# Kernel optimization log

Measured on AMD Instinct MI355X. Metric: run time of the kernel, lower is better.

Reference implementation:

```python
import jax, jax.numpy as jnp
from jax import lax
import numpy as np

N = 10000      # nodes
E = 160000     # edges (avg degree 16)
IN = 128       # in_channels
H = 64         # hidden_channels
OUT = 112      # out_channels
L = 28         # num GENConv layers
LN_EPS = 1e-5
MSG_EPS = 1e-7   # GENConv adds eps after relu in message
SM_EPS = 1e-16   # PyG scatter-softmax denominator eps


def _ln(x, g, b):
    mu = jnp.mean(x, axis=-1, keepdims=True)
    var = jnp.mean(jnp.square(x - mu), axis=-1, keepdims=True)
    return (x - mu) * lax.rsqrt(var + LN_EPS) * g + b


def setup_inputs() -> dict:
    key = jax.random.key(0)
    ks = jax.random.split(key, 8)

    def w(k, shape, fan_in):
        return (jax.random.normal(k, shape, dtype=jnp.float32) / np.float32(np.sqrt(fan_in)))

    x = jax.random.normal(ks[0], (N, IN), dtype=jnp.float32)
    edge_index = jax.random.randint(ks[1], (2, E), 0, N, dtype=jnp.int32)

    inp = {
        "x": x,
        "edge_index": edge_index,
        # node encoder
        "enc_W": w(ks[2], (IN, H), IN),
        "enc_b": jnp.zeros((H,), jnp.float32),
        # per-layer DeepGCNLayer LayerNorm (res+ pre-norm)
        "ln_g": jnp.ones((L, H), jnp.float32),
        "ln_b": jnp.zeros((L, H), jnp.float32),
        # per-layer learnable softmax temperature t (init 1.0)
        "t": jnp.ones((L,), jnp.float32),
        # GENConv inner MLP: Linear(H,2H) -> LayerNorm -> ReLU -> Linear(2H,H)
        "W1": w(ks[3], (L, H, 2 * H), H),
        "b1": jnp.zeros((L, 2 * H), jnp.float32),
        "mlp_g": jnp.ones((L, 2 * H), jnp.float32),
        "mlp_b": jnp.zeros((L, 2 * H), jnp.float32),
        "W2": w(ks[4], (L, 2 * H, H), 2 * H),
        "b2": jnp.zeros((L, H), jnp.float32),
        # output head
        "head_W": w(ks[5], (H, OUT), H),
        "head_b": jnp.zeros((OUT,), jnp.float32),
    }
    return inp


def reference(x, edge_index, enc_W, enc_b, ln_g, ln_b, t, W1, b1,
              mlp_g, mlp_b, W2, b2, head_W, head_b):
    src, dst = edge_index[0], edge_index[1]
    n = x.shape[0]

    h = x @ enc_W + enc_b  # node encoder

    def layer(h, params):
        lg, lb, tt, w1, bb1, mg, mb, w2, bb2 = params
        # DeepGCNLayer 'res+': norm -> act -> (dropout: identity at eval) -> conv -> residual
        z = jax.nn.relu(_ln(h, lg, lb))  # [N,H]
        # GENConv message: relu(x_j) + eps   (no edge_attr)
        m = jax.nn.relu(z[src]) + MSG_EPS  # [E,H]
        # softmax aggregation per destination node, per channel, temperature t
        logits = m * tt
        mx = jax.ops.segment_max(logits, dst, num_segments=n)  # [N,H]
        mx = jnp.where(jnp.isfinite(mx), mx, 0.0)              # empty segments
        ex = jnp.exp(logits - mx[dst])
        den = jax.ops.segment_sum(ex, dst, num_segments=n)
        alpha = ex / (den[dst] + SM_EPS)
        agg = jax.ops.segment_sum(alpha * m, dst, num_segments=n)  # [N,H]
        # GENConv: out = mlp(x_r + aggr)
        out = agg + z
        u = jax.nn.relu(_ln(out @ w1 + bb1, mg, mb))
        u = u @ w2 + bb2
        return h + u, None  # residual

    h, _ = lax.scan(layer, h, (ln_g, ln_b, t, W1, b1, mlp_g, mlp_b, W2, b2))
    return h @ head_W + head_b  # [N,OUT]
```

## Files before the change

### kernel.cpp

```cpp
#include <hip/hip_runtime.h>

#define N_NODES 10000
#define N_EDGES 160000
#define IN_CH 128
#define H 64
#define H2 128
#define OUT_CH 112
#define NLAYERS 28

__global__ __launch_bounds__(256) void k_count(const int* __restrict__ ei, int* __restrict__ deg) {
  int e = blockIdx.x * 256 + threadIdx.x;
  atomicAdd(&deg[ei[N_EDGES + e]], 1);
}

__global__ __launch_bounds__(1024) void k_scan(const int* __restrict__ deg, int* __restrict__ offs) {
  __shared__ int sums[1024];
  constexpr int CH = 10;
  int t = threadIdx.x;
  int base = t * CH;
  int local[CH];
  int s = 0;
  #pragma unroll
  for (int i = 0; i < CH; i++) {
    int idx = base + i;
    int v = (idx < N_NODES) ? deg[idx] : 0;
    local[i] = s; s += v;
  }
  sums[t] = s;
  __syncthreads();
  for (int off = 1; off < 1024; off <<= 1) {
    int v = (t >= off) ? sums[t - off] : 0;
    __syncthreads();
    sums[t] += v;
    __syncthreads();
  }
  int prev = (t == 0) ? 0 : sums[t - 1];
  #pragma unroll
  for (int i = 0; i < CH; i++) {
    int idx = base + i;
    if (idx < N_NODES) offs[idx] = prev + local[i];
  }
  if (t == 1023) offs[N_NODES] = sums[1023];
}

__global__ __launch_bounds__(256) void k_fill(const int* __restrict__ ei, const int* __restrict__ offs,
                                              int* __restrict__ cur, int* __restrict__ csr) {
  int e = blockIdx.x * 256 + threadIdx.x;
  int d = ei[N_EDGES + e];
  int p = offs[d] + atomicAdd(&cur[d], 1);
  csr[p] = ei[e];
}

__global__ __launch_bounds__(256) void k_pack(const float* __restrict__ W1, const float* __restrict__ W2,
                                              float* __restrict__ W1P, float* __restrict__ W2P) {
  int l = blockIdx.x;
  const float* w1 = W1 + l * 8192; float* p1 = W1P + l * 8192;
  const float* w2 = W2 + l * 8192; float* p2 = W2P + l * 8192;
  int t = threadIdx.x;
  for (int i = t; i < 8192; i += 256) {
    int g = i >> 9, r = i & 511;
    int lane = r >> 3, j = (r >> 1) & 3, c = r & 1;
    p1[i] = w1[(4 * g + j) * H2 + lane * 2 + c];
  }
  for (int i = t; i < 8192; i += 256) {
    int g = i >> 8, r = i & 255;
    int lane = r >> 2, j = r & 3;
    p2[i] = w2[(4 * g + j) * H + lane];
  }
}

__global__ __launch_bounds__(256) void k_encoder(
    const float* __restrict__ x, const float* __restrict__ Wenc, const float* __restrict__ benc,
    const float* __restrict__ lng, const float* __restrict__ lnb,
    float* __restrict__ h, float* __restrict__ z) {
  __shared__ float Xs[8][IN_CH];
  int t = threadIdx.x;
  int tile = blockIdx.x * 8;
  {
    int r = t >> 5, c4 = t & 31;
    float4 v = ((const float4*)x)[(tile + r) * 32 + c4];
    *(float4*)&Xs[r][c4 * 4] = v;
  }
  __syncthreads();
  int lane = t & 63;
  int wave = __builtin_amdgcn_readfirstlane(t >> 6);
  int n0 = wave * 2;
  float b = benc[lane];
  float a0 = b, a1 = b;
  #pragma unroll
  for (int k = 0; k < IN_CH; k += 4) {
    float4 X0 = *(float4*)&Xs[n0][k];
    float4 X1 = *(float4*)&Xs[n0 + 1][k];
    float w0 = Wenc[(k + 0) * H + lane];
    float w1 = Wenc[(k + 1) * H + lane];
    float w2 = Wenc[(k + 2) * H + lane];
    float w3 = Wenc[(k + 3) * H + lane];
    a0 = fmaf(X0.x, w0, a0); a0 = fmaf(X0.y, w1, a0); a0 = fmaf(X0.z, w2, a0); a0 = fmaf(X0.w, w3, a0);
    a1 = fmaf(X1.x, w0, a1); a1 = fmaf(X1.y, w1, a1); a1 = fmaf(X1.z, w2, a1); a1 = fmaf(X1.w, w3, a1);
  }
  float g = lng[lane], bb = lnb[lane];
  #pragma unroll
  for (int i = 0; i < 2; i++) {
    float a = (i == 0) ? a0 : a1;
    float s = a, q = a * a;
    #pragma unroll
    for (int m = 1; m < 64; m <<= 1) { s += __shfl_xor(s, m); q += __shfl_xor(q, m); }
    float mu = s * (1.0f / 64.0f);
    float var = q * (1.0f / 64.0f) - mu * mu;
    float rs = rsqrtf(var + 1e-5f);
    int gn = tile + n0 + i;
    h[gn * H + lane] = a;
    z[gn * H + lane] = fmaxf(fmaf((a - mu) * rs, g, bb), 0.f);
  }
}

__global__ __launch_bounds__(256) void k_layer(
    const float* __restrict__ zc, float* __restrict__ zn, float* __restrict__ h,
    const int* __restrict__ offs, const int* __restrict__ csr,
    const float* __restrict__ tvec,
    const float* __restrict__ W1P, const float* __restrict__ b1,
    const float* __restrict__ mg, const float* __restrict__ mb,
    const float* __restrict__ W2P, const float* __restrict__ b2,
    const float* __restrict__ lngn, const float* __restrict__ lnbn,
    int l) {
  __shared__ float As[8][H];
  __shared__ float Us[8][H2];
  int t = threadIdx.x;
  int lane = t & 63;
  int wave = __builtin_amdgcn_readfirstlane(t >> 6);
  int nb0 = blockIdx.x * 8 + wave * 2;

  float tl = tvec[l] * 1.44269504088896340736f;
  #pragma unroll
  for (int i = 0; i < 2; i++) {
    int gn = nb0 + i;
    int e0 = offs[gn], e1 = offs[gn + 1];
    float d0 = 0.f, d1 = 0.f, d2 = 0.f, d3 = 0.f;
    float a0 = 0.f, a1 = 0.f, a2 = 0.f, a3 = 0.f;
    int e = e0;
    for (; e + 4 <= e1; e += 4) {
      int s0 = csr[e], s1 = csr[e + 1], s2 = csr[e + 2], s3 = csr[e + 3];
      float v0 = zc[s0 * H + lane] + 1e-7f;
      float v1 = zc[s1 * H + lane] + 1e-7f;
      float v2 = zc[s2 * H + lane] + 1e-7f;
      float v3 = zc[s3 * H + lane] + 1e-7f;
      float p0 = exp2f(v0 * tl), p1 = exp2f(v1 * tl);
      float p2 = exp2f(v2 * tl), p3 = exp2f(v3 * tl);
      d0 += p0; d1 += p1; d2 += p2; d3 += p3;
      a0 = fmaf(p0, v0, a0); a1 = fmaf(p1, v1, a1);
      a2 = fmaf(p2, v2, a2); a3 = fmaf(p3, v3, a3);
    }
    for (; e < e1; e++) {
      int s0 = csr[e];
      float v0 = zc[s0 * H + lane] + 1e-7f;
      float p0 = exp2f(v0 * tl);
      d0 += p0; a0 = fmaf(p0, v0, a0);
    }
    float den = (d0 + d1) + (d2 + d3);
    float acc = (a0 + a1) + (a2 + a3);
    As[wave * 2 + i][lane] = acc / (den + 1e-16f) + zc[gn * H + lane];
  }
  __syncthreads();

  {
    const float* W1Pl = W1P + (size_t)l * (H * H2);
    const float* b1l = b1 + l * H2;
    int c0 = lane * 2;
    float bb0 = b1l[c0], bb1 = b1l[c0 + 1];
    float u00 = bb0, u01 = bb1, u10 = bb0, u11 = bb1;
    #pragma unroll
    for (int g = 0; g < 16; g++) {
      float4 A0 = *(float4*)&As[wave * 2 + 0][g * 4];
      float4 A1 = *(float4*)&As[wave * 2 + 1][g * 4];
      float4 wa = *(const float4*)&W1Pl[g * 512 + lane * 8];
      float4 wb = *(const float4*)&W1Pl[g * 512 + lane * 8 + 4];
      u00 = fmaf(A0.x, wa.x, u00); u01 = fmaf(A0.x, wa.y, u01);
      u00 = fmaf(A0.y, wa.z, u00); u01 = fmaf(A0.y, wa.w, u01);
      u00 = fmaf(A0.z, wb.x, u00); u01 = fmaf(A0.z, wb.y, u01);
      u00 = fmaf(A0.w, wb.z, u00); u01 = fmaf(A0.w, wb.w, u01);
      u10 = fmaf(A1.x, wa.x, u10); u11 = fmaf(A1.x, wa.y, u11);
      u10 = fmaf(A1.y, wa.z, u10); u11 = fmaf(A1.y, wa.w, u11);
      u10 = fmaf(A1.z, wb.x, u10); u11 = fmaf(A1.z, wb.y, u11);
      u10 = fmaf(A1.w, wb.z, u10); u11 = fmaf(A1.w, wb.w, u11);
    }
    float s0 = u00 + u01, q0 = u00 * u00 + u01 * u01;
    float s1 = u10 + u11, q1 = u10 * u10 + u11 * u11;
    #pragma unroll
    for (int m = 1; m < 64; m <<= 1) {
      s0 += __shfl_xor(s0, m); q0 += __shfl_xor(q0, m);
      s1 += __shfl_xor(s1, m); q1 += __shfl_xor(q1, m);
    }
    float mu0 = s0 * (1.0f / 128.0f), mu1 = s1 * (1.0f / 128.0f);
    float rs0 = rsqrtf(q0 * (1.0f / 128.0f) - mu0 * mu0 + 1e-5f);
    float rs1 = rsqrtf(q1 * (1.0f / 128.0f) - mu1 * mu1 + 1e-5f);
    const float* mgl = mg + l * H2;
    const float* mbl = mb + l * H2;
    float g0 = mgl[c0], g1 = mgl[c0 + 1], h0 = mbl[c0], h1 = mbl[c0 + 1];
    float o00 = fmaxf(fmaf((u00 - mu0) * rs0, g0, h0), 0.f);
    float o01 = fmaxf(fmaf((u01 - mu0) * rs0, g1, h1), 0.f);
    float o10 = fmaxf(fmaf((u10 - mu1) * rs1, g0, h0), 0.f);
    float o11 = fmaxf(fmaf((u11 - mu1) * rs1, g1, h1), 0.f);
    *(float2*)&Us[wave * 2 + 0][c0] = make_float2(o00, o01);
    *(float2*)&Us[wave * 2 + 1][c0] = make_float2(o10, o11);
  }
  __syncthreads();

  {
    const float* W2Pl = W2P + (size_t)l * (H2 * H);
    const float* b2l = b2 + l * H;
    float bb = b2l[lane];
    float v0 = bb, v1 = bb;
    #pragma unroll
    for (int g = 0; g < 32; g++) {
      float4 X0 = *(float4*)&Us[wave * 2 + 0][g * 4];
      float4 X1 = *(float4*)&Us[wave * 2 + 1][g * 4];
      float4 w = *(const float4*)&W2Pl[g * 256 + lane * 4];
      v0 = fmaf(X0.x, w.x, v0); v0 = fmaf(X0.y, w.y, v0);
      v0 = fmaf(X0.z, w.z, v0); v0 = fmaf(X0.w, w.w, v0);
      v1 = fmaf(X1.x, w.x, v1); v1 = fmaf(X1.y, w.y, v1);
      v1 = fmaf(X1.z, w.z, v1); v1 = fmaf(X1.w, w.w, v1);
    }
    float g = lngn[lane], bgn = lnbn[lane];
    #pragma unroll
    for (int i = 0; i < 2; i++) {
      int gn = nb0 + i;
      float add = (i == 0) ? v0 : v1;
      float hv = h[gn * H + lane] + add;
      h[gn * H + lane] = hv;
      if (l != NLAYERS - 1) {
        float s = hv, q = hv * hv;
        #pragma unroll
        for (int m = 1; m < 64; m <<= 1) { s += __shfl_xor(s, m); q += __shfl_xor(q, m); }
        float mu = s * (1.0f / 64.0f);
        float var = q * (1.0f / 64.0f) - mu * mu;
        float rs = rsqrtf(var + 1e-5f);
        zn[gn * H + lane] = fmaxf(fmaf((hv - mu) * rs, g, bgn), 0.f);
      }
    }
  }
}

__global__ __launch_bounds__(256) void k_head(const float* __restrict__ h, const float* __restrict__ Wh,
                                              const float* __restrict__ bh, float* __restrict__ out) {
  __shared__ float Hs[8][H];
  int t = threadIdx.x;
  int tile = blockIdx.x * 8;
  if (t < 128) {
    int r = t >> 4, c4 = t & 15;
    float4 v = ((const float4*)h)[(tile + r) * 16 + c4];
    *(float4*)&Hs[r][c4 * 4] = v;
  }
  __syncthreads();
  int lane = t & 63;
  int wave = __builtin_amdgcn_readfirstlane(t >> 6);
  int n0 = wave * 2;
  int c2 = 64 + ((lane < 48) ? lane : 47);
  float b0 = bh[lane], b1 = bh[c2];
  float a00 = b0, a01 = b1, a10 = b0, a11 = b1;
  #pragma unroll
  for (int k = 0; k < H; k += 4) {
    float4 X0 = *(float4*)&Hs[n0][k];
    float4 X1 = *(float4*)&Hs[n0 + 1][k];
    float wA0 = Wh[(k + 0) * OUT_CH + lane], wB0 = Wh[(k + 0) * OUT_CH + c2];
    float wA1 = Wh[(k + 1) * OUT_CH + lane], wB1 = Wh[(k + 1) * OUT_CH + c2];
    float wA2 = Wh[(k + 2) * OUT_CH + lane], wB2 = Wh[(k + 2) * OUT_CH + c2];
    float wA3 = Wh[(k + 3) * OUT_CH + lane], wB3 = Wh[(k + 3) * OUT_CH + c2];
    a00 = fmaf(X0.x, wA0, a00); a01 = fmaf(X0.x, wB0, a01);
    a00 = fmaf(X0.y, wA1, a00); a01 = fmaf(X0.y, wB1, a01);
    a00 = fmaf(X0.z, wA2, a00); a01 = fmaf(X0.z, wB2, a01);
    a00 = fmaf(X0.w, wA3, a00); a01 = fmaf(X0.w, wB3, a01);
    a10 = fmaf(X1.x, wA0, a10); a11 = fmaf(X1.x, wB0, a11);
    a10 = fmaf(X1.y, wA1, a10); a11 = fmaf(X1.y, wB1, a11);
    a10 = fmaf(X1.z, wA2, a10); a11 = fmaf(X1.z, wB2, a11);
    a10 = fmaf(X1.w, wA3, a10); a11 = fmaf(X1.w, wB3, a11);
  }
  int gn0 = tile + n0;
  out[gn0 * OUT_CH + lane] = a00;
  out[(gn0 + 1) * OUT_CH + lane] = a10;
  if (lane < 48) {
    out[gn0 * OUT_CH + 64 + lane] = a01;
    out[(gn0 + 1) * OUT_CH + 64 + lane] = a11;
  }
}

extern "C" void kernel_launch(void* const* d_in, const int* in_sizes, int n_in,
                              void* d_out, int out_size, void* d_ws, size_t ws_size,
                              hipStream_t stream) {
  (void)in_sizes; (void)n_in; (void)out_size; (void)ws_size;
  const float* x    = (const float*)d_in[0];
  const int*   ei   = (const int*)d_in[1];
  const float* encW = (const float*)d_in[2];
  const float* encb = (const float*)d_in[3];
  const float* lng  = (const float*)d_in[4];
  const float* lnb  = (const float*)d_in[5];
  const float* tv   = (const float*)d_in[6];
  const float* W1   = (const float*)d_in[7];
  const float* b1   = (const float*)d_in[8];
  const float* mg   = (const float*)d_in[9];
  const float* mb   = (const float*)d_in[10];
  const float* W2   = (const float*)d_in[11];
  const float* b2   = (const float*)d_in[12];
  const float* Wh   = (const float*)d_in[13];
  const float* bh   = (const float*)d_in[14];

  char* ws = (char*)d_ws;
  int*   deg  = (int*)(ws + 0);
  int*   cur  = (int*)(ws + 40000);
  int*   offs = (int*)(ws + 80000);
  int*   csr  = (int*)(ws + 120064);
  float* h    = (float*)(ws + 760064);
  float* z0   = (float*)(ws + 3320064);
  float* z1   = (float*)(ws + 5880064);
  float* W1P  = (float*)(ws + 8440064);
  float* W2P  = (float*)(ws + 9357568);

  hipMemsetAsync(ws, 0, 80000, stream);
  k_count<<<625, 256, 0, stream>>>(ei, deg);
  k_pack<<<28, 256, 0, stream>>>(W1, W2, W1P, W2P);
  k_scan<<<1, 1024, 0, stream>>>(deg, offs);
  k_fill<<<625, 256, 0, stream>>>(ei, offs, cur, csr);
  k_encoder<<<1250, 256, 0, stream>>>(x, encW, encb, lng, lnb, h, z0);

  float* zc = z0;
  float* znx = z1;
  for (int l = 0; l < NLAYERS; l++) {
    int ln_next = (l + 1 < NLAYERS) ? (l + 1) : l;
    k_layer<<<1250, 256, 0, stream>>>(zc, znx, h, offs, csr, tv,
                                      W1P, b1, mg, mb, W2P, b2,
                                      lng + ln_next * H, lnb + ln_next * H, l);
    float* tmp = zc; zc = znx; znx = tmp;
  }
  k_head<<<1250, 256, 0, stream>>>(h, Wh, bh, (float*)d_out);
}
```

Baseline: 636.6 us.

## Split layer into aggregation and MLP kernels with LDS-staged swizzled weights

Splits the fused per-layer kernel into a gather/softmax-aggregation kernel (one node per wave, 2500 blocks) and an MLP kernel that stages both layer weight matrices (64KB) in shared memory with a swizzled W1 layout and handles 16 nodes per block (4 per wave). The aim is to reuse weights from LDS across more nodes instead of re-reading them from global or L2 per pair of nodes, and to give the latency-bound gather more parallelism. In exchange it adds an extra launch per layer and a global round trip of the aggregated features. The 64KB of LDS per block also limits how many blocks can be resident per CU.

```diff
diff --git a/kernel.cpp b/kernel.cpp
--- a/kernel.cpp
+++ b/kernel.cpp
@@ -51,21 +51,34 @@
   csr[p] = ei[e];
 }
 
+__device__ __forceinline__ int w1_off(int g, int lane, int h) {
+  int col = (2 * (lane & 3) + h + (lane >> 2)) & 7;
+  return (g * 128 + (lane >> 2) * 8 + col) * 4;
+}
+
 __global__ __launch_bounds__(256) void k_pack(const float* __restrict__ W1, const float* __restrict__ W2,
-                                              float* __restrict__ W1P, float* __restrict__ W2P) {
+                                              float* __restrict__ WP) {
   int l = blockIdx.x;
-  const float* w1 = W1 + l * 8192; float* p1 = W1P + l * 8192;
-  const float* w2 = W2 + l * 8192; float* p2 = W2P + l * 8192;
-  int t = threadIdx.x;
-  for (int i = t; i < 8192; i += 256) {
-    int g = i >> 9, r = i & 511;
-    int lane = r >> 3, j = (r >> 1) & 3, c = r & 1;
-    p1[i] = w1[(4 * g + j) * H2 + lane * 2 + c];
-  }
-  for (int i = t; i < 8192; i += 256) {
-    int g = i >> 8, r = i & 255;
-    int lane = r >> 2, j = r & 3;
-    p2[i] = w2[(4 * g + j) * H + lane];
+  const float* w1 = W1 + l * 8192;
+  const float* w2 = W2 + l * 8192;
+  float* p = WP + (size_t)l * 16384;
+  int t = threadIdx.x;
+  for (int i = t; i < 2048; i += 256) {
+    int g = i >> 7, r = i & 127;
+    int lane = r >> 1, hh = r & 1;
+    int off = w1_off(g, lane, hh);
+    #pragma unroll
+    for (int e = 0; e < 4; e++) {
+      int j = hh * 2 + (e >> 1), c = e & 1;
+      p[off + e] = w1[(4 * g + j) * H2 + lane * 2 + c];
+    }
+  }
+  for (int i = t; i < 2048; i += 256) {
+    int g = i >> 6, lane = i & 63;
+    int off = 8192 + i * 4;
+    #pragma unroll
+    for (int j = 0; j < 4; j++)
+      p[off + j] = w2[(4 * g + j) * H + lane];
   }
 }
 
@@ -114,127 +127,149 @@
   }
 }
 
-__global__ __launch_bounds__(256) void k_layer(
-    const float* __restrict__ zc, float* __restrict__ zn, float* __restrict__ h,
-    const int* __restrict__ offs, const int* __restrict__ csr,
-    const float* __restrict__ tvec,
-    const float* __restrict__ W1P, const float* __restrict__ b1,
+__global__ __launch_bounds__(256) void k_agg(
+    const float* __restrict__ zc, const int* __restrict__ offs, const int* __restrict__ csr,
+    const float* __restrict__ tvec, float* __restrict__ As, int l) {
+  int t = threadIdx.x;
+  int lane = t & 63;
+  int gn = blockIdx.x * 4 + (t >> 6);
+  float tl = tvec[l] * 1.44269504088896340736f;
+  int e0 = offs[gn], e1 = offs[gn + 1];
+  float d0 = 0.f, d1 = 0.f, d2 = 0.f, d3 = 0.f;
+  float a0 = 0.f, a1 = 0.f, a2 = 0.f, a3 = 0.f;
+  int e = e0;
+  for (; e + 4 <= e1; e += 4) {
+    int s0 = csr[e], s1 = csr[e + 1], s2 = csr[e + 2], s3 = csr[e + 3];
+    float v0 = zc[s0 * H + lane] + 1e-7f;
+    float v1 = zc[s1 * H + lane] + 1e-7f;
+    float v2 = zc[s2 * H + lane] + 1e-7f;
+    float v3 = zc[s3 * H + lane] + 1e-7f;
+    float p0 = exp2f(v0 * tl), p1 = exp2f(v1 * tl);
+    float p2 = exp2f(v2 * tl), p3 = exp2f(v3 * tl);
+    d0 += p0; d1 += p1; d2 += p2; d3 += p3;
+    a0 = fmaf(p0, v0, a0); a1 = fmaf(p1, v1, a1);
+    a2 = fmaf(p2, v2, a2); a3 = fmaf(p3, v3, a3);
+  }
+  for (; e < e1; e++) {
+    int s0 = csr[e];
+    float v0 = zc[s0 * H + lane] + 1e-7f;
+    float p0 = exp2f(v0 * tl);
+    d0 += p0; a0 = fmaf(p0, v0, a0);
+  }
+  float den = (d0 + d1) + (d2 + d3);
+  float acc = (a0 + a1) + (a2 + a3);
+  As[gn * H + lane] = acc / (den + 1e-16f) + zc[gn * H + lane];
+}
+
+__global__ __launch_bounds__(256) void k_mlp(
+    const float* __restrict__ As_g, float* __restrict__ zn, float* __restrict__ h,
+    const float* __restrict__ WP, const float* __restrict__ b1,
     const float* __restrict__ mg, const float* __restrict__ mb,
-    const float* __restrict__ W2P, const float* __restrict__ b2,
+    const float* __restrict__ b2,
     const float* __restrict__ lngn, const float* __restrict__ lnbn,
-    int l) {
-  __shared__ float As[8][H];
-  __shared__ float Us[8][H2];
+    int l, int last) {
+  __shared__ float Ws[16384];
+  __shared__ float Asl[16][H];
+  __shared__ float Us[16][H2];
   int t = threadIdx.x;
   int lane = t & 63;
   int wave = __builtin_amdgcn_readfirstlane(t >> 6);
-  int nb0 = blockIdx.x * 8 + wave * 2;
-
-  float tl = tvec[l] * 1.44269504088896340736f;
-  #pragma unroll
-  for (int i = 0; i < 2; i++) {
-    int gn = nb0 + i;
-    int e0 = offs[gn], e1 = offs[gn + 1];
-    float d0 = 0.f, d1 = 0.f, d2 = 0.f, d3 = 0.f;
-    float a0 = 0.f, a1 = 0.f, a2 = 0.f, a3 = 0.f;
-    int e = e0;
-    for (; e + 4 <= e1; e += 4) {
-      int s0 = csr[e], s1 = csr[e + 1], s2 = csr[e + 2], s3 = csr[e + 3];
-      float v0 = zc[s0 * H + lane] + 1e-7f;
-      float v1 = zc[s1 * H + lane] + 1e-7f;
-      float v2 = zc[s2 * H + lane] + 1e-7f;
-      float v3 = zc[s3 * H + lane] + 1e-7f;
-      float p0 = exp2f(v0 * tl), p1 = exp2f(v1 * tl);
-      float p2 = exp2f(v2 * tl), p3 = exp2f(v3 * tl);
-      d0 += p0; d1 += p1; d2 += p2; d3 += p3;
-      a0 = fmaf(p0, v0, a0); a1 = fmaf(p1, v1, a1);
-      a2 = fmaf(p2, v2, a2); a3 = fmaf(p3, v3, a3);
-    }
-    for (; e < e1; e++) {
-      int s0 = csr[e];
-      float v0 = zc[s0 * H + lane] + 1e-7f;
-      float p0 = exp2f(v0 * tl);
-      d0 += p0; a0 = fmaf(p0, v0, a0);
-    }
-    float den = (d0 + d1) + (d2 + d3);
-    float acc = (a0 + a1) + (a2 + a3);
-    As[wave * 2 + i][lane] = acc / (den + 1e-16f) + zc[gn * H + lane];
-  }
-  __syncthreads();
-
+  int tile = blockIdx.x * 16;
+
+  const float* WPl = WP + (size_t)l * 16384;
+  #pragma unroll
+  for (int i = 0; i < 16; i++) {
+    float4 v = *(const float4*)&WPl[(i * 256 + t) * 4];
+    *(float4*)&Ws[(i * 256 + t) * 4] = v;
+  }
   {
-    const float* W1Pl = W1P + (size_t)l * (H * H2);
+    int r = t >> 4, c = (t & 15) * 4;
+    *(float4*)&Asl[r][c] = *(const float4*)&As_g[(tile + r) * H + c];
+  }
+  __syncthreads();
+
+  int n0 = wave * 4;
+  {
     const float* b1l = b1 + l * H2;
     int c0 = lane * 2;
     float bb0 = b1l[c0], bb1 = b1l[c0 + 1];
-    float u00 = bb0, u01 = bb1, u10 = bb0, u11 = bb1;
+    float u0[4], u1[4];
+    #pragma unroll
+    for (int i = 0; i < 4; i++) { u0[i] = bb0; u1[i] = bb1; }
+    int lb = (lane >> 2) * 8;
+    int cA = (2 * (lane & 3) + 0 + (lane >> 2)) & 7;
+    int cB = (2 * (lane & 3) + 1 + (lane >> 2)) & 7;
     #pragma unroll
     for (int g = 0; g < 16; g++) {
-      float4 A0 = *(float4*)&As[wave * 2 + 0][g * 4];
-      float4 A1 = *(float4*)&As[wave * 2 + 1][g * 4];
-      float4 wa = *(const float4*)&W1Pl[g * 512 + lane * 8];
-      float4 wb = *(const float4*)&W1Pl[g * 512 + lane * 8 + 4];
-      u00 = fmaf(A0.x, wa.x, u00); u01 = fmaf(A0.x, wa.y, u01);
-      u00 = fmaf(A0.y, wa.z, u00); u01 = fmaf(A0.y, wa.w, u01);
-      u00 = fmaf(A0.z, wb.x, u00); u01 = fmaf(A0.z, wb.y, u01);
-      u00 = fmaf(A0.w, wb.z, u00); u01 = fmaf(A0.w, wb.w, u01);
-      u10 = fmaf(A1.x, wa.x, u10); u11 = fmaf(A1.x, wa.y, u11);
-      u10 = fmaf(A1.y, wa.z, u10); u11 = fmaf(A1.y, wa.w, u11);
-      u10 = fmaf(A1.z, wb.x, u10); u11 = fmaf(A1.z, wb.y, u11);
-      u10 = fmaf(A1.w, wb.z, u10); u11 = fmaf(A1.w, wb.w, u11);
-    }
-    float s0 = u00 + u01, q0 = u00 * u00 + u01 * u01;
-    float s1 = u10 + u11, q1 = u10 * u10 + u11 * u11;
+      float4 wa = *(float4*)&Ws[(g * 128 + lb + cA) * 4];
+      float4 wb = *(float4*)&Ws[(g * 128 + lb + cB) * 4];
+      #pragma unroll
+      for (int i = 0; i < 4; i++) {
+        float4 A = *(float4*)&Asl[n0 + i][g * 4];
+        u0[i] = fmaf(A.x, wa.x, u0[i]); u1[i] = fmaf(A.x, wa.y, u1[i]);
+        u0[i] = fmaf(A.y, wa.z, u0[i]); u1[i] = fmaf(A.y, wa.w, u1[i]);
+        u0[i] = fmaf(A.z, wb.x, u0[i]); u1[i] = fmaf(A.z, wb.y, u1[i]);
+        u0[i] = fmaf(A.w, wb.z, u0[i]); u1[i] = fmaf(A.w, wb.w, u1[i]);
+      }
+    }
+    float s[4], q[4];
+    #pragma unroll
+    for (int i = 0; i < 4; i++) { s[i] = u0[i] + u1[i]; q[i] = u0[i] * u0[i] + u1[i] * u1[i]; }
     #pragma unroll
     for (int m = 1; m < 64; m <<= 1) {
-      s0 += __shfl_xor(s0, m); q0 += __shfl_xor(q0, m);
-      s1 += __shfl_xor(s1, m); q1 += __shfl_xor(q1, m);
-    }
-    float mu0 = s0 * (1.0f / 128.0f), mu1 = s1 * (1.0f / 128.0f);
-    float rs0 = rsqrtf(q0 * (1.0f / 128.0f) - mu0 * mu0 + 1e-5f);
-    float rs1 = rsqrtf(q1 * (1.0f / 128.0f) - mu1 * mu1 + 1e-5f);
+      #pragma unroll
+      for (int i = 0; i < 4; i++) { s[i] += __shfl_xor(s[i], m); q[i] += __shfl_xor(q[i], m); }
+    }
     const float* mgl = mg + l * H2;
     const float* mbl = mb + l * H2;
-    float g0 = mgl[c0], g1 = mgl[c0 + 1], h0 = mbl[c0], h1 = mbl[c0 + 1];
-    float o00 = fmaxf(fmaf((u00 - mu0) * rs0, g0, h0), 0.f);
-    float o01 = fmaxf(fmaf((u01 - mu0) * rs0, g1, h1), 0.f);
-    float o10 = fmaxf(fmaf((u10 - mu1) * rs1, g0, h0), 0.f);
-    float o11 = fmaxf(fmaf((u11 - mu1) * rs1, g1, h1), 0.f);
-    *(float2*)&Us[wave * 2 + 0][c0] = make_float2(o00, o01);
-    *(float2*)&Us[wave * 2 + 1][c0] = make_float2(o10, o11);
+    float g0 = mgl[c0], g1 = mgl[c0 + 1], hb0 = mbl[c0], hb1 = mbl[c0 + 1];
+    #pragma unroll
+    for (int i = 0; i < 4; i++) {
+      float mu = s[i] * (1.0f / 128.0f);
+      float rs = rsqrtf(q[i] * (1.0f / 128.0f) - mu * mu + 1e-5f);
+      float o0 = fmaxf(fmaf((u0[i] - mu) * rs, g0, hb0), 0.f);
+      float o1 = fmaxf(fmaf((u1[i] - mu) * rs, g1, hb1), 0.f);
+      *(float2*)&Us[n0 + i][c0] = make_float2(o0, o1);
+    }
   }
   __syncthreads();
 
   {
-    const float* W2Pl = W2P + (size_t)l * (H2 * H);
     const float* b2l = b2 + l * H;
     float bb = b2l[lane];
-    float v0 = bb, v1 = bb;
+    float v[4];
+    #pragma unroll
+    for (int i = 0; i < 4; i++) v[i] = bb;
     #pragma unroll
     for (int g = 0; g < 32; g++) {
-      float4 X0 = *(float4*)&Us[wave * 2 + 0][g * 4];
-      float4 X1 = *(float4*)&Us[wave * 2 + 1][g * 4];
-      float4 w = *(const float4*)&W2Pl[g * 256 + lane * 4];
-      v0 = fmaf(X0.x, w.x, v0); v0 = fmaf(X0.y, w.y, v0);
-      v0 = fmaf(X0.z, w.z, v0); v0 = fmaf(X0.w, w.w, v0);
-      v1 = fmaf(X1.x, w.x, v1); v1 = fmaf(X1.y, w.y, v1);
-      v1 = fmaf(X1.z, w.z, v1); v1 = fmaf(X1.w, w.w, v1);
-    }
-    float g = lngn[lane], bgn = lnbn[lane];
-    #pragma unroll
-    for (int i = 0; i < 2; i++) {
-      int gn = nb0 + i;
-      float add = (i == 0) ? v0 : v1;
-      float hv = h[gn * H + lane] + add;
-      h[gn * H + lane] = hv;
-      if (l != NLAYERS - 1) {
-        float s = hv, q = hv * hv;
+      float4 w = *(float4*)&Ws[8192 + (g * 64 + lane) * 4];
+      #pragma unroll
+      for (int i = 0; i < 4; i++) {
+        float4 X = *(float4*)&Us[n0 + i][g * 4];
+        v[i] = fmaf(X.x, w.x, v[i]); v[i] = fmaf(X.y, w.y, v[i]);
+        v[i] = fmaf(X.z, w.z, v[i]); v[i] = fmaf(X.w, w.w, v[i]);
+      }
+    }
+    float hv[4], s[4], q[4];
+    #pragma unroll
+    for (int i = 0; i < 4; i++) {
+      int gn = tile + n0 + i;
+      hv[i] = h[gn * H + lane] + v[i];
+      h[gn * H + lane] = hv[i];
+      s[i] = hv[i]; q[i] = hv[i] * hv[i];
+    }
+    if (!last) {
+      #pragma unroll
+      for (int m = 1; m < 64; m <<= 1) {
         #pragma unroll
-        for (int m = 1; m < 64; m <<= 1) { s += __shfl_xor(s, m); q += __shfl_xor(q, m); }
-        float mu = s * (1.0f / 64.0f);
-        float var = q * (1.0f / 64.0f) - mu * mu;
-        float rs = rsqrtf(var + 1e-5f);
-        zn[gn * H + lane] = fmaxf(fmaf((hv - mu) * rs, g, bgn), 0.f);
+        for (int i = 0; i < 4; i++) { s[i] += __shfl_xor(s[i], m); q[i] += __shfl_xor(q[i], m); }
+      }
+      float gg = lngn[lane], gb = lnbn[lane];
+      #pragma unroll
+      for (int i = 0; i < 4; i++) {
+        float mu = s[i] * (1.0f / 64.0f);
+        float rs = rsqrtf(q[i] * (1.0f / 64.0f) - mu * mu + 1e-5f);
+        zn[(tile + n0 + i) * H + lane] = fmaxf(fmaf((hv[i] - mu) * rs, gg, gb), 0.f);
       }
     }
   }
@@ -311,12 +346,12 @@
   float* h    = (float*)(ws + 760064);
   float* z0   = (float*)(ws + 3320064);
   float* z1   = (float*)(ws + 5880064);
-  float* W1P  = (float*)(ws + 8440064);
-  float* W2P  = (float*)(ws + 9357568);
+  float* As   = (float*)(ws + 8440064);
+  float* WP   = (float*)(ws + 11000064);
 
   hipMemsetAsync(ws, 0, 80000, stream);
   k_count<<<625, 256, 0, stream>>>(ei, deg);
-  k_pack<<<28, 256, 0, stream>>>(W1, W2, W1P, W2P);
+  k_pack<<<28, 256, 0, stream>>>(W1, W2, WP);
   k_scan<<<1, 1024, 0, stream>>>(deg, offs);
   k_fill<<<625, 256, 0, stream>>>(ei, offs, cur, csr);
   k_encoder<<<1250, 256, 0, stream>>>(x, encW, encb, lng, lnb, h, z0);
@@ -325,9 +360,10 @@
   float* znx = z1;
   for (int l = 0; l < NLAYERS; l++) {
     int ln_next = (l + 1 < NLAYERS) ? (l + 1) : l;
-    k_layer<<<1250, 256, 0, stream>>>(zc, znx, h, offs, csr, tv,
-                                      W1P, b1, mg, mb, W2P, b2,
-                                      lng + ln_next * H, lnb + ln_next * H, l);
+    k_agg<<<2500, 256, 0, stream>>>(zc, offs, csr, tv, As, l);
+    k_mlp<<<625, 256, 0, stream>>>(As, znx, h, WP, b1, mg, mb, b2,
+                                   lng + ln_next * H, lnb + ln_next * H,
+                                   l, (l == NLAYERS - 1) ? 1 : 0);
     float* tmp = zc; zc = znx; znx = tmp;
   }
   k_head<<<1250, 256, 0, stream>>>(h, Wh, bh, (float*)d_out);
```

Measured after the change: 849.8 us. 1.33x slower.
